# Kernel optimization log

Hardware: AMD Instinct MI355X
Metric: run time of the kernel (lower is better)

The kernel has to match this reference:

```python
import jax, jax.numpy as jnp
import numpy as np
import math

B, S, D, K = 8, 2048, 1024, 64
EPS = 1e-5

def _ln(x):
    m = jnp.mean(x, axis=-1, keepdims=True)
    v = jnp.mean((x - m) ** 2, axis=-1, keepdims=True)
    return (x - m) * jax.lax.rsqrt(v + EPS)

def setup_inputs() -> dict:
    key = jax.random.key(0)
    ks = jax.random.split(key, 14)
    s = 0.02
    return {
        "x":  jax.random.normal(ks[0], (B, S, D), dtype=jnp.float32),
        "Wk": jax.random.normal(ks[1], (D, K), dtype=jnp.float32) * s,
        "bk": jnp.zeros((K,), dtype=jnp.float32),
        "Wq": jax.random.normal(ks[2], (D, K), dtype=jnp.float32) * s,
        "bq": jnp.zeros((K,), dtype=jnp.float32),
        "Wv": jax.random.normal(ks[3], (D, D), dtype=jnp.float32) * s,
        "bv": jnp.zeros((D,), dtype=jnp.float32),
        "Wb": jax.random.normal(ks[4], (D, 1), dtype=jnp.float32) * s,
        "bb": jnp.zeros((1,), dtype=jnp.float32),
        "W1": jax.random.normal(ks[5], (D, D), dtype=jnp.float32) * s,
        "b1": jnp.zeros((D,), dtype=jnp.float32),
        "g1": jnp.ones((D,), dtype=jnp.float32),
        "be1": jnp.zeros((D,), dtype=jnp.float32),
    }

def reference(x, Wk, bk, Wq, bq, Wv, bv, Wb, bb, W1, b1, g1, be1):
    scale = 1.0 / math.sqrt(K)
    keys    = (jnp.einsum('bsd,dk->bsk', x, Wk) + bk) * scale   # [B,S,K]
    queries = jnp.einsum('bsd,dk->bsk', x, Wq) + bq             # [B,S,K]
    values  = jnp.einsum('bsd,de->bse', x, Wv) + bv             # [B,S,D]
    biases  = jnp.einsum('bsd,do->bso', x, Wb) + bb             # [B,S,1]
    # scores[b,i,j] = keys[b,i] . queries[b,j] + biases[b,i]
    scores = jax.nn.sigmoid(jnp.einsum('bik,bjk->bij', keys, queries) + biases)
    attention = jnp.einsum('bij,bjd->bid', scores, values)      # [B,S,D]
    res = _ln(x + attention) * g1 + be1
    feedforward = jax.nn.relu(jnp.einsum('bsd,de->bse', res, W1) + b1)
    return _ln(res + feedforward)
```

## Files before the change

### kernel.cpp

```cpp
#include <hip/hip_runtime.h>
#include <math.h>


typedef __bf16 bf16_t;
typedef __bf16 bf16x4_t __attribute__((ext_vector_type(4)));
typedef __bf16 bf16x8_t __attribute__((ext_vector_type(8)));
typedef float  f32x4    __attribute__((ext_vector_type(4)));

#define DEV static __device__ __forceinline__

DEV void gll16(const void* g, void* l) {
  __builtin_amdgcn_global_load_lds(
      (const __attribute__((address_space(1))) void*)g,
      (__attribute__((address_space(3))) void*)l, 16, 0, 0);
}

template <int MODE, int MFAST>
__global__ __launch_bounds__(512, 4) void gemm128n(
    const bf16_t* __restrict__ A, const bf16_t* __restrict__ B,
    bf16_t* __restrict__ C, int K, int lda, int ldb, int ldc,
    const float* __restrict__ aux0) {
  const int gx = gridDim.x, gy = gridDim.y;
  const int nwg = gx * gy;
  const int orig = blockIdx.x + gx * blockIdx.y;
  const int lid = (orig & 7) * (nwg >> 3) + (orig >> 3);
  const int bx = MFAST ? (lid / gy) : (lid % gx);
  const int by = MFAST ? (lid % gy) : (lid / gx);
  const int m0 = by * 256, n0 = bx * 128;

  __shared__ bf16_t SM[24576];
#define ASH(s) (&SM[(s) << 13])
#define BSH(s) (&SM[16384 + ((s) << 12)])

  const int tid = threadIdx.x;
  const int wid = tid >> 6, l = tid & 63;
  const int wr = wid >> 1, wc = wid & 1;
  const int lr = l & 15, lh = l >> 4;

  const int sRow = tid >> 2;
  const int sSl = (tid & 3) ^ ((tid >> 3) & 3);
  const bf16_t* Asrc = A + (long)(m0 + sRow) * lda + sSl * 8;
  const bf16_t* Bsrc = B + (long)(n0 + sRow) * ldb + sSl * 8;
  const long aStep = (long)128 * lda;

  const int sw = (lh ^ ((lr >> 1) & 3)) * 8;
  const int aOff = (wr * 64 + lr) * 32 + sw;
  const int bOff = (wc * 64 + lr) * 32 + sw;

  f32x4 acc[4][4] = {};
  const int NT = K >> 5;

  gll16(Asrc, ASH(0) + tid * 8);
  gll16(Asrc + aStep, ASH(0) + 4096 + tid * 8);
  gll16(Bsrc, BSH(0) + tid * 8);

  for (int h = 0; h < NT; ++h) {
    const int s = h & 1;
    asm volatile("s_waitcnt vmcnt(0)" ::: "memory");
    __builtin_amdgcn_sched_barrier(0);
    __builtin_amdgcn_s_barrier();
    if (h + 1 < NT) {
      const bf16_t* a_ = Asrc + (h + 1) * 32;
      const bf16_t* b_ = Bsrc + (h + 1) * 32;
      gll16(a_, ASH(s ^ 1) + tid * 8);
      gll16(a_ + aStep, ASH(s ^ 1) + 4096 + tid * 8);
      gll16(b_, BSH(s ^ 1) + tid * 8);
    }
    bf16x8_t aF[4], bF[4];
#pragma unroll
    for (int m = 0; m < 4; ++m) aF[m] = *(const bf16x8_t*)(ASH(s) + aOff + m * 512);
#pragma unroll
    for (int n = 0; n < 4; ++n) bF[n] = *(const bf16x8_t*)(BSH(s) + bOff + n * 512);
    asm volatile("s_waitcnt lgkmcnt(0)" ::: "memory");
    __builtin_amdgcn_sched_barrier(0);
    __builtin_amdgcn_s_setprio(1);
#pragma unroll
    for (int m = 0; m < 4; ++m)
#pragma unroll
      for (int n = 0; n < 4; ++n)
        acc[m][n] = __builtin_amdgcn_mfma_f32_16x16x32_bf16(aF[m], bF[n], acc[m][n], 0, 0, 0);
    __builtin_amdgcn_s_setprio(0);
  }

  const int rowb = m0 + wr * 64 + lh * 4;
  const int colb = n0 + wc * 64 + lr;
#pragma unroll
  for (int m = 0; m < 4; ++m)
#pragma unroll
    for (int n = 0; n < 4; ++n) {
      const f32x4 v = acc[m][n];
      const int cc = colb + n * 16;
#pragma unroll
      for (int r = 0; r < 4; ++r) {
        const int rr = rowb + m * 16 + r;
        const float val = v[r];
        if constexpr (MODE == 1) {
          C[(long)rr * ldc + cc] = (bf16_t)(val + aux0[rr]);
        } else {
          C[(long)rr * ldc + cc] = (bf16_t)fmaxf(val + aux0[cc], 0.0f);
        }
      }
    }
#undef ASH
#undef BSH
}

template <int MODE>
__global__ __launch_bounds__(512, 2) void gemm256p(
    const bf16_t* __restrict__ A, const bf16_t* __restrict__ B,
    bf16_t* __restrict__ C, int K, int lda, int ldb, int ldc,
    long sAb, long sBb, long sCb, const float* __restrict__ aux0) {
  const int gx = gridDim.x, gy = gridDim.y;
  const int gxy = gx * gy;
  const int nwg = gxy * (int)gridDim.z;
  const int orig = blockIdx.x + gx * blockIdx.y + gxy * blockIdx.z;
  const int lid = (orig & 7) * (nwg >> 3) + (orig >> 3);
  const int bz = lid / gxy;
  const int rem = lid - bz * gxy;
  const int bx = rem % gx;
  const int by = rem / gx;

  A += (long)bz * sAb;
  B += (long)bz * sBb;
  const int m0 = by * 256, n0 = bx * 256;

  __shared__ bf16_t SM[65536];
#define ASH(b, h) (&SM[(((b)*2 + (h)) << 13)])
#define BSH(b, h) (&SM[32768 + (((b)*2 + (h)) << 13)])

  const int tid = threadIdx.x;
  const int wid = tid >> 6, l = tid & 63;
  const int wr = wid >> 2, wc = wid & 3;
  const int lr = l & 15, lh = l >> 4;

  const int sRow = tid >> 2;
  const int sSl = (tid & 3) ^ ((tid >> 3) & 3);
  const bf16_t* Asrc = A + (long)(m0 + sRow) * lda + sSl * 8;
  const bf16_t* Bsrc = B + (long)(n0 + sRow) * ldb + sSl * 8;
  const long aStep = (long)128 * lda, bStep = (long)128 * ldb;

#define STAGE_A(b, h, kt) do { \
    const bf16_t* s_ = Asrc + (kt) * 64 + (h) * 32; \
    gll16(s_,         ASH(b, h) + tid * 8); \
    gll16(s_ + aStep, ASH(b, h) + 4096 + tid * 8); } while (0)
#define STAGE_B(b, h, kt) do { \
    const bf16_t* s_ = Bsrc + (kt) * 64 + (h) * 32; \
    gll16(s_,         BSH(b, h) + tid * 8); \
    gll16(s_ + bStep, BSH(b, h) + 4096 + tid * 8); } while (0)

  const int sw = (lh ^ ((lr >> 1) & 3)) * 8;
  const int aOff = (wr * 128 + lr) * 32 + sw;
  const int bOff = (wc * 64 + lr) * 32 + sw;

  f32x4 acc[8][4] = {};
  const int NT = K >> 6;

#define LGKM(n) do { \
    asm volatile("s_waitcnt lgkmcnt(" #n ")" ::: "memory"); \
    __builtin_amdgcn_sched_barrier(0); } while (0)
#define MFMA16(AS, BS, mo) do { \
    __builtin_amdgcn_s_setprio(1); \
    _Pragma("unroll") for (int m = 0; m < 4; ++m) \
    _Pragma("unroll") for (int n = 0; n < 4; ++n) \
      acc[m + (mo)][n] = __builtin_amdgcn_mfma_f32_16x16x32_bf16(AS[m], BS[n], acc[m + (mo)][n], 0, 0, 0); \
    __builtin_amdgcn_s_setprio(0); } while (0)

  STAGE_A(0, 0, 0); STAGE_B(0, 0, 0); STAGE_A(0, 1, 0); STAGE_B(0, 1, 0);
  asm volatile("s_waitcnt vmcnt(4)" ::: "memory");
  __builtin_amdgcn_s_barrier();

  bf16x8_t aA[4], aB[4], bA[4], bB[4];
#pragma unroll
  for (int n = 0; n < 4; ++n) bA[n] = *(const bf16x8_t*)(BSH(0, 0) + bOff + n * 512);
#pragma unroll
  for (int m = 0; m < 4; ++m) aA[m] = *(const bf16x8_t*)(ASH(0, 0) + aOff + m * 512);

  for (int t = 0; t < NT; ++t) {
    const int p = t & 1, q = p ^ 1;
    const bool pf = (t + 1 < NT);

#pragma unroll
    for (int m = 0; m < 4; ++m) aB[m] = *(const bf16x8_t*)(ASH(p, 0) + aOff + (m + 4) * 512);
    if (pf) STAGE_A(q, 0, t + 1);
    LGKM(4);
    MFMA16(aA, bA, 0);

    if (pf) {
      asm volatile("s_waitcnt vmcnt(2)" ::: "memory");
    } else {
      asm volatile("s_waitcnt vmcnt(0)" ::: "memory");
    }
    __builtin_amdgcn_sched_barrier(0);
    __builtin_amdgcn_s_barrier();
#pragma unroll
    for (int m = 0; m < 4; ++m) aA[m] = *(const bf16x8_t*)(ASH(p, 1) + aOff + m * 512);
#pragma unroll
    for (int n = 0; n < 4; ++n) bB[n] = *(const bf16x8_t*)(BSH(p, 1) + bOff + n * 512);
    if (pf) STAGE_B(q, 0, t + 1);
    LGKM(8);
    MFMA16(aB, bA, 4);

#pragma unroll
    for (int m = 0; m < 4; ++m) aB[m] = *(const bf16x8_t*)(ASH(p, 1) + aOff + (m + 4) * 512);
    if (pf) STAGE_A(q, 1, t + 1);
    LGKM(4);
    MFMA16(aA, bB, 0);

    if (pf) STAGE_B(q, 1, t + 1);
    asm volatile("s_waitcnt lgkmcnt(0)" ::: "memory");
    if (pf) {
      asm volatile("s_waitcnt vmcnt(4)" ::: "memory");
    }
    __builtin_amdgcn_sched_barrier(0);
    __builtin_amdgcn_s_barrier();
    if (pf) {
#pragma unroll
      for (int n = 0; n < 4; ++n) bA[n] = *(const bf16x8_t*)(BSH(q, 0) + bOff + n * 512);
#pragma unroll
      for (int m = 0; m < 4; ++m) aA[m] = *(const bf16x8_t*)(ASH(q, 0) + aOff + m * 512);
    }
    __builtin_amdgcn_sched_barrier(0);
    MFMA16(aB, bB, 4);
  }
#undef STAGE_A
#undef STAGE_B
#undef LGKM
#undef MFMA16

  bf16_t* Cb = C + (long)bz * sCb;
  const int rowb = m0 + wr * 128 + lh * 4;
  const int colb = n0 + wc * 64 + lr;
#pragma unroll
  for (int m = 0; m < 8; ++m)
#pragma unroll
    for (int n = 0; n < 4; ++n) {
      const f32x4 v = acc[m][n];
      const int cc = colb + n * 16;
#pragma unroll
      for (int r = 0; r < 4; ++r) {
        const int rr = rowb + m * 16 + r;
        Cb[(long)rr * ldc + cc] = (bf16_t)v[r];
      }
    }
#undef ASH
#undef BSH
}

__global__ __launch_bounds__(256) void scores128(
    const bf16_t* __restrict__ kq, bf16_t* __restrict__ C,
    const float* __restrict__ biases) {
  const int orig = blockIdx.x + 16 * blockIdx.y + 256 * blockIdx.z;
  const int lid = (orig & 7) * 256 + (orig >> 3);
  const int bz = lid >> 8;
  const int rem = lid & 255;
  const int bx = rem & 15, by = rem >> 4;

  const bf16_t* A = kq + (long)bz * 2048 * 128;
  const bf16_t* B = A + 64;
  const float* a0 = biases + (long)bz * 2048;
  const int m0 = by * 128, n0 = bx * 128;

  __shared__ bf16_t SM[16384];
#define ASH(h) (&SM[(h) << 12])
#define BSH(h) (&SM[8192 + ((h) << 12)])

  const int tid = threadIdx.x;
  const int w = tid >> 6, l = tid & 63;
  const int wr = w >> 1, wc = w & 1;
  const int lr = l & 15, lh = l >> 4;

  const int sRow = tid >> 2;
  const int sSl = ((tid & 3) ^ ((tid >> 3) & 3)) * 8;
  const bf16_t* As = A + (long)(m0 + sRow) * 128 + sSl;
  const bf16_t* Bs = B + (long)(n0 + sRow) * 128 + sSl;
#pragma unroll
  for (int h = 0; h < 2; ++h) {
    gll16(As + h * 32, ASH(h) + tid * 8);
    gll16(As + h * 32 + 64 * 128, ASH(h) + 2048 + tid * 8);
    gll16(Bs + h * 32, BSH(h) + tid * 8);
    gll16(Bs + h * 32 + 64 * 128, BSH(h) + 2048 + tid * 8);
  }
  asm volatile("s_waitcnt vmcnt(0)" ::: "memory");
  __builtin_amdgcn_s_barrier();

  const int sw = (lh ^ ((lr >> 1) & 3)) * 8;
  const int aOff = (wr * 64 + lr) * 32 + sw;
  const int bOff = (wc * 64 + lr) * 32 + sw;

  f32x4 acc[4][4] = {};
#pragma unroll
  for (int h = 0; h < 2; ++h) {
    bf16x8_t aF[4], bF[4];
#pragma unroll
    for (int m = 0; m < 4; ++m) aF[m] = *(const bf16x8_t*)(ASH(h) + aOff + m * 512);
#pragma unroll
    for (int n = 0; n < 4; ++n) bF[n] = *(const bf16x8_t*)(BSH(h) + bOff + n * 512);
#pragma unroll
    for (int m = 0; m < 4; ++m)
#pragma unroll
      for (int n = 0; n < 4; ++n)
        acc[m][n] = __builtin_amdgcn_mfma_f32_16x16x32_bf16(aF[m], bF[n], acc[m][n], 0, 0, 0);
  }

  __builtin_amdgcn_s_barrier();
  {
    const int rowb = (wr << 6) + (lh << 2);
    const int colb = (wc << 6) + lr;
#pragma unroll
    for (int m = 0; m < 4; ++m)
#pragma unroll
      for (int n = 0; n < 4; ++n) {
        const f32x4 v = acc[m][n];
        const int cl = colb + (n << 4);
#pragma unroll
        for (int r = 0; r < 4; ++r) {
          const int rl = rowb + (m << 4) + r;
          const float zz = v[r] + a0[m0 + rl];
          SM[rl * 128 + (cl ^ (lh << 4))] =
              (bf16_t)__builtin_amdgcn_rcpf(1.0f + __expf(-zz));
        }
      }
    __syncthreads();
    bf16_t* Cb = C + (long)bz * 2048 * 2048;
    const int chunk = tid & 15, rsub = tid >> 4;
#pragma unroll
    for (int pp = 0; pp < 8; ++pp) {
      const int rl = pp * 16 + rsub;
      const int sc = chunk ^ (((rl >> 2) & 3) << 1);
      const bf16x8_t vv = *(const bf16x8_t*)&SM[rl * 128 + sc * 8];
      *(bf16x8_t*)&Cb[(long)(m0 + rl) * 2048 + n0 + chunk * 8] = vv;
    }
  }
#undef ASH
#undef BSH
}

__global__ __launch_bounds__(256) void kq_thin(
    const bf16_t* __restrict__ A, const bf16_t* __restrict__ B,
    bf16_t* __restrict__ C,
    const float* __restrict__ bk, const float* __restrict__ bq) {
  const int m0 = blockIdx.x * 64;

  __shared__ bf16_t SM[12288];
#define ASH(b) (&SM[(b) << 11])
#define BSH(b) (&SM[4096 + ((b) << 12)])

  const int tid = threadIdx.x;
  const int w = tid >> 6, l = tid & 63;
  const int lr = l & 15, lh = l >> 4;

  const int sRow = tid >> 2;
  const int sSl = (tid & 3) ^ ((tid >> 3) & 3);
  const bf16_t* Asrc = A + (long)(m0 + sRow) * 1024 + sSl * 8;
  const bf16_t* Bsrc0 = B + (long)sRow * 1024 + sSl * 8;
  const bf16_t* Bsrc1 = B + (long)(64 + sRow) * 1024 + sSl * 8;

  const int sw = (lh ^ ((lr >> 1) & 3)) * 8;
  const int aOff = (w * 16 + lr) * 32 + sw;

  f32x4 acc[8] = {};

  auto stage = [&](int buf, int k0) {
    gll16(Asrc + k0, ASH(buf) + tid * 8);
    gll16(Bsrc0 + k0, BSH(buf) + tid * 8);
    gll16(Bsrc1 + k0, BSH(buf) + 2048 + tid * 8);
  };

  stage(0, 0);
  __syncthreads();
  int cur = 0;

  for (int k0 = 0; k0 < 1024; k0 += 32) {
    if (k0 + 32 < 1024) stage(cur ^ 1, k0 + 32);

    const bf16x8_t aF = *(const bf16x8_t*)(ASH(cur) + aOff);
    bf16x8_t bF[8];
#pragma unroll
    for (int j = 0; j < 8; ++j)
      bF[j] = *(const bf16x8_t*)(BSH(cur) + (j * 16 + lr) * 32 + sw);
#pragma unroll
    for (int j = 0; j < 8; ++j)
      acc[j] = __builtin_amdgcn_mfma_f32_16x16x32_bf16(aF, bF[j], acc[j], 0, 0, 0);

    __syncthreads();
    cur ^= 1;
  }

  {
#pragma unroll
    for (int j = 0; j < 8; ++j) {
      const f32x4 v = acc[j];
      const int cl = j * 16 + lr;
      const float b = (cl < 64) ? bk[cl] : bq[cl - 64];
      const float s = (cl < 64) ? 0.125f : 1.0f;
#pragma unroll
      for (int r = 0; r < 4; ++r) {
        const int rl = w * 16 + lh * 4 + r;
        SM[rl * 128 + (cl ^ (lh << 4))] = (bf16_t)((v[r] + b) * s);
      }
    }
    __syncthreads();
    const int chunk = tid & 15, rsub = tid >> 4;
#pragma unroll
    for (int pp = 0; pp < 4; ++pp) {
      const int rl = pp * 16 + rsub;
      const int sc = chunk ^ (((rl >> 2) & 3) << 1);
      const bf16x8_t vv = *(const bf16x8_t*)&SM[rl * 128 + sc * 8];
      *(bf16x8_t*)&C[(long)(m0 + rl) * 128 + chunk * 8] = vv;
    }
  }
#undef ASH
#undef BSH
}

__global__ __launch_bounds__(256) void cast_bias_kernel(
    const float* __restrict__ x, const float* __restrict__ Wb,
    const float* __restrict__ bb, bf16_t* __restrict__ x_bf,
    float* __restrict__ biases) {
  const int r = blockIdx.x * 4 + (threadIdx.x >> 6);
  const int l = threadIdx.x & 63;
  const float* xr = x + (long)r * 1024;
  bf16_t* orow = x_bf + (long)r * 1024;
  float s = 0.f;
#pragma unroll
  for (int i = 0; i < 4; ++i) {
    const int off = l * 4 + i * 256;
    const float4 v = *(const float4*)(xr + off);
    const float4 w = *(const float4*)(Wb + off);
    s += v.x * w.x + v.y * w.y + v.z * w.z + v.w * w.w;
    bf16x4_t o;
    o[0] = (bf16_t)v.x; o[1] = (bf16_t)v.y; o[2] = (bf16_t)v.z; o[3] = (bf16_t)v.w;
    *(bf16x4_t*)(orow + off) = o;
  }
#pragma unroll
  for (int off = 1; off < 64; off <<= 1) s += __shfl_xor(s, off);
  if (l == 0) biases[r] = s + bb[0];
}

__global__ __launch_bounds__(256) void transpose_all(
    const float* __restrict__ Wk, const float* __restrict__ Wq,
    const float* __restrict__ Wv, const float* __restrict__ W1,
    bf16_t* __restrict__ Wkqt, bf16_t* __restrict__ Wvt,
    bf16_t* __restrict__ W1t) {
  int b = blockIdx.x;
  const float* in;
  bf16_t* out;
  int R, C, c0, r0;
  if (b < 1024) {
    in = Wv; out = Wvt; R = 1024; C = 1024;
    c0 = (b & 31) * 32; r0 = (b >> 5) * 32;
  } else if (b < 2048) {
    b -= 1024; in = W1; out = W1t; R = 1024; C = 1024;
    c0 = (b & 31) * 32; r0 = (b >> 5) * 32;
  } else if (b < 2112) {
    b -= 2048; in = Wk; out = Wkqt; R = 1024; C = 64;
    c0 = (b & 1) * 32; r0 = (b >> 1) * 32;
  } else {
    b -= 2112; in = Wq; out = Wkqt + 64 * 1024; R = 1024; C = 64;
    c0 = (b & 1) * 32; r0 = (b >> 1) * 32;
  }
  __shared__ float t[32][33];
  const int tx = threadIdx.x & 31, ty = threadIdx.x >> 5;
#pragma unroll
  for (int i = 0; i < 4; ++i) {
    const int rl = ty * 4 + i;
    t[rl][tx] = in[(long)(r0 + rl) * C + c0 + tx];
  }
  __syncthreads();
#pragma unroll
  for (int i = 0; i < 4; ++i) {
    const int rl = ty * 4 + i;
    out[(long)(c0 + rl) * R + r0 + tx] = (bf16_t)t[tx][rl];
  }
}

__global__ __launch_bounds__(256) void ln1_kernel(
    const bf16_t* __restrict__ x, const bf16_t* __restrict__ attn,
    const float* __restrict__ g, const float* __restrict__ be,
    bf16_t* __restrict__ res) {
  const int w = threadIdx.x >> 6, l = threadIdx.x & 63;
  const long r = (long)blockIdx.x * 4 + w;
  const bf16_t* xr = x + r * 1024;
  const bf16_t* ar = attn + r * 1024;
  float y[16];
  float s = 0.f, ss = 0.f;
#pragma unroll
  for (int h = 0; h < 2; ++h) {
    const int base = h * 512 + l * 8;
    const bf16x8_t xv = *(const bf16x8_t*)(xr + base);
    const bf16x8_t av = *(const bf16x8_t*)(ar + base);
#pragma unroll
    for (int j = 0; j < 8; ++j) {
      const float yy = (float)xv[j] + (float)av[j];
      y[h * 8 + j] = yy;
      s += yy; ss += yy * yy;
    }
  }
#pragma unroll
  for (int off = 1; off < 64; off <<= 1) {
    s += __shfl_xor(s, off);
    ss += __shfl_xor(ss, off);
  }
  const float mean = s * (1.0f / 1024.0f);
  const float rs = rsqrtf(ss * (1.0f / 1024.0f) - mean * mean + 1e-5f);
  bf16_t* orow = res + r * 1024;
#pragma unroll
  for (int h = 0; h < 2; ++h) {
    const int base = h * 512 + l * 8;
    bf16x8_t o;
#pragma unroll
    for (int j = 0; j < 8; ++j)
      o[j] = (bf16_t)((y[h * 8 + j] - mean) * rs * g[base + j] + be[base + j]);
    *(bf16x8_t*)(orow + base) = o;
  }
}

__global__ __launch_bounds__(256) void ln2_kernel(
    const bf16_t* __restrict__ res, const bf16_t* __restrict__ hh,
    float* __restrict__ out) {
  const int w = threadIdx.x >> 6, l = threadIdx.x & 63;
  const long r = (long)blockIdx.x * 4 + w;
  const bf16_t* rr = res + r * 1024;
  const bf16_t* hr = hh + r * 1024;
  float y[16];
  float s = 0.f, ss = 0.f;
#pragma unroll
  for (int h = 0; h < 2; ++h) {
    const int base = h * 512 + l * 8;
    const bf16x8_t rv = *(const bf16x8_t*)(rr + base);
    const bf16x8_t hv = *(const bf16x8_t*)(hr + base);
#pragma unroll
    for (int j = 0; j < 8; ++j) {
      const float yy = (float)rv[j] + (float)hv[j];
      y[h * 8 + j] = yy;
      s += yy; ss += yy * yy;
    }
  }
#pragma unroll
  for (int off = 1; off < 64; off <<= 1) {
    s += __shfl_xor(s, off);
    ss += __shfl_xor(ss, off);
  }
  const float mean = s * (1.0f / 1024.0f);
  const float rs = rsqrtf(ss * (1.0f / 1024.0f) - mean * mean + 1e-5f);
  float* orow = out + r * 1024;
#pragma unroll
  for (int h = 0; h < 2; ++h) {
    const int base = h * 512 + l * 8;
    float4 o1, o2;
    o1.x = (y[h * 8 + 0] - mean) * rs; o1.y = (y[h * 8 + 1] - mean) * rs;
    o1.z = (y[h * 8 + 2] - mean) * rs; o1.w = (y[h * 8 + 3] - mean) * rs;
    o2.x = (y[h * 8 + 4] - mean) * rs; o2.y = (y[h * 8 + 5] - mean) * rs;
    o2.z = (y[h * 8 + 6] - mean) * rs; o2.w = (y[h * 8 + 7] - mean) * rs;
    *(float4*)(orow + base) = o1;
    *(float4*)(orow + base + 4) = o2;
  }
}

extern "C" void kernel_launch(void* const* d_in, const int* in_sizes, int n_in,
                              void* d_out, int out_size, void* d_ws, size_t ws_size,
                              hipStream_t stream) {
  const float* x   = (const float*)d_in[0];
  const float* Wk  = (const float*)d_in[1];
  const float* bk  = (const float*)d_in[2];
  const float* Wq  = (const float*)d_in[3];
  const float* bq  = (const float*)d_in[4];
  const float* Wv  = (const float*)d_in[5];
  const float* bv  = (const float*)d_in[6];
  const float* Wb  = (const float*)d_in[7];
  const float* bb  = (const float*)d_in[8];
  const float* W1  = (const float*)d_in[9];
  const float* b1  = (const float*)d_in[10];
  const float* g1  = (const float*)d_in[11];
  const float* be1 = (const float*)d_in[12];
  float* out = (float*)d_out;

  char* ws = (char*)d_ws;
  bf16_t* x_bf    = (bf16_t*)(ws + 0);
  bf16_t* vt_bf   = (bf16_t*)(ws + 33554432);
  bf16_t* kq_bf   = (bf16_t*)(ws + 67108864);
  bf16_t* Wkqt    = (bf16_t*)(ws + 71303168);
  bf16_t* Wvt     = (bf16_t*)(ws + 71565312);
  bf16_t* W1t     = (bf16_t*)(ws + 73662464);
  float*  biases  = (float*) (ws + 75759616);
  bf16_t* scores  = (bf16_t*)(ws + 75825152);
  bf16_t* attn_bf = (bf16_t*)(ws + 142934016);
  bf16_t* res_bf  = (bf16_t*)(ws + 176488448);
  bf16_t* h_bf    = attn_bf;

  cast_bias_kernel<<<4096, 256, 0, stream>>>(x, Wb, bb, x_bf, biases);
  transpose_all<<<2176, 256, 0, stream>>>(Wk, Wq, Wv, W1, Wkqt, Wvt, W1t);

  kq_thin<<<256, 256, 0, stream>>>(x_bf, Wkqt, kq_bf, bk, bq);

  gemm128n<1, 1><<<dim3(128, 4), 512, 0, stream>>>(
      Wvt, x_bf, vt_bf, 1024, 1024, 1024, 16384, bv);

  scores128<<<dim3(16, 16, 8), 256, 0, stream>>>(kq_bf, scores, biases);

  gemm256p<3><<<dim3(4, 8, 8), 512, 0, stream>>>(
      scores, vt_bf, attn_bf, 2048, 2048, 16384, 1024,
      2048L * 2048, 2048, 2048L * 1024, nullptr);

  ln1_kernel<<<4096, 256, 0, stream>>>(x_bf, attn_bf, g1, be1, res_bf);

  gemm128n<4, 0><<<dim3(8, 64), 512, 0, stream>>>(
      res_bf, W1t, h_bf, 1024, 1024, 1024, 1024, b1);

  ln2_kernel<<<4096, 256, 0, stream>>>(res_bf, h_bf, out);
}
```

Baseline: 235.5 us.

## Fuse feed-forward GEMM with final LayerNorm and merge prep kernels

```diff
diff --git a/kernel.cpp b/kernel.cpp
--- a/kernel.cpp
+++ b/kernel.cpp
@@ -13,6 +13,122 @@
   __builtin_amdgcn_global_load_lds(
       (const __attribute__((address_space(1))) void*)g,
       (__attribute__((address_space(3))) void*)l, 16, 0, 0);
+}
+
+__global__ __launch_bounds__(512, 2) void ff_rowln(
+    const bf16_t* __restrict__ A, const bf16_t* __restrict__ B,
+    const float* __restrict__ b1, float* __restrict__ out) {
+  const int m0 = blockIdx.x * 64;
+
+  __shared__ bf16_t SM[69632];
+#define ASH(s) (&SM[(s) << 11])
+#define BSH(s) (&SM[4096 + ((s) << 15)])
+  float* SM32 = (float*)SM;
+
+  const int tid = threadIdx.x;
+  const int wc = tid >> 6, l = tid & 63;
+  const int lr = l & 15, lh = l >> 4;
+
+  const int gRow = tid >> 2;
+  const int gSl = ((tid & 3) ^ ((tid >> 3) & 3)) * 8;
+  const bf16_t* Asrc = A + (long)(m0 + gRow) * 1024 + gSl;
+  const bf16_t* Bsrc = B + (long)gRow * 1024 + gSl;
+
+  const int sw = (lh ^ ((lr >> 1) & 3)) * 8;
+
+  f32x4 acc[4][8] = {};
+
+#define STAGE(s, kt) do { \
+    if (tid < 256) gll16(Asrc + (kt) * 32, ASH(s) + tid * 8); \
+    _Pragma("unroll") for (int r = 0; r < 8; ++r) \
+      gll16(Bsrc + (long)r * 131072 + (kt) * 32, BSH(s) + (r * 512 + tid) * 8); \
+  } while (0)
+
+  STAGE(0, 0);
+  for (int kt = 0; kt < 32; ++kt) {
+    const int s = kt & 1;
+    asm volatile("s_waitcnt vmcnt(0)" ::: "memory");
+    __builtin_amdgcn_sched_barrier(0);
+    __builtin_amdgcn_s_barrier();
+    if (kt + 1 < 32) STAGE(s ^ 1, kt + 1);
+    bf16x8_t aF[4], bF[8];
+#pragma unroll
+    for (int m = 0; m < 4; ++m)
+      aF[m] = *(const bf16x8_t*)(ASH(s) + (m * 16 + lr) * 32 + sw);
+#pragma unroll
+    for (int n = 0; n < 8; ++n)
+      bF[n] = *(const bf16x8_t*)(BSH(s) + (wc * 128 + n * 16 + lr) * 32 + sw);
+    asm volatile("s_waitcnt lgkmcnt(0)" ::: "memory");
+    __builtin_amdgcn_sched_barrier(0);
+    __builtin_amdgcn_s_setprio(1);
+#pragma unroll
+    for (int m = 0; m < 4; ++m)
+#pragma unroll
+      for (int n = 0; n < 8; ++n)
+        acc[m][n] = __builtin_amdgcn_mfma_f32_16x16x32_bf16(aF[m], bF[n], acc[m][n], 0, 0, 0);
+    __builtin_amdgcn_s_setprio(0);
+  }
+#undef STAGE
+
+  const int ecol0 = wc * 128 + lr;
+#pragma unroll
+  for (int half = 0; half < 2; ++half) {
+    __builtin_amdgcn_s_barrier();
+#pragma unroll
+    for (int mm = 0; mm < 2; ++mm) {
+#pragma unroll
+      for (int n = 0; n < 8; ++n) {
+        const int col = ecol0 + n * 16;
+        const float bb = b1[col];
+        const f32x4 v = acc[half * 2 + mm][n];
+#pragma unroll
+        for (int r = 0; r < 4; ++r) {
+          const int row32 = mm * 16 + lh * 4 + r;
+          const int chunk = (col >> 2) ^ (row32 & 15);
+          SM32[row32 * 1024 + chunk * 4 + (col & 3)] = fmaxf(v[r] + bb, 0.f);
+        }
+      }
+    }
+    __builtin_amdgcn_s_barrier();
+    const int row = tid >> 4, seg = tid & 15;
+    const long grow = m0 + half * 32 + row;
+    const bf16_t* resp = A + grow * 1024 + seg * 64;
+    float y[64];
+    float s = 0.f, ss = 0.f;
+#pragma unroll
+    for (int j = 0; j < 8; ++j) {
+      const bf16x8_t rv = *(const bf16x8_t*)(resp + j * 8);
+      const int c0 = seg * 16 + 2 * j;
+      const f32x4 h0 = *(const f32x4*)&SM32[row * 1024 + ((c0 ^ (row & 15)) << 2)];
+      const f32x4 h1 = *(const f32x4*)&SM32[row * 1024 + (((c0 + 1) ^ (row & 15)) << 2)];
+#pragma unroll
+      for (int k = 0; k < 4; ++k) {
+        const float y0 = h0[k] + (float)rv[k];
+        y[j * 8 + k] = y0; s += y0; ss += y0 * y0;
+        const float y1 = h1[k] + (float)rv[4 + k];
+        y[j * 8 + 4 + k] = y1; s += y1; ss += y1 * y1;
+      }
+    }
+#pragma unroll
+    for (int off = 1; off < 16; off <<= 1) {
+      s += __shfl_xor(s, off);
+      ss += __shfl_xor(ss, off);
+    }
+    const float mean = s * (1.0f / 1024.0f);
+    const float rstd = rsqrtf(ss * (1.0f / 1024.0f) - mean * mean + 1e-5f);
+    float4* op = (float4*)(out + grow * 1024 + seg * 64);
+#pragma unroll
+    for (int j = 0; j < 16; ++j) {
+      float4 o;
+      o.x = (y[j * 4 + 0] - mean) * rstd;
+      o.y = (y[j * 4 + 1] - mean) * rstd;
+      o.z = (y[j * 4 + 2] - mean) * rstd;
+      o.w = (y[j * 4 + 3] - mean) * rstd;
+      op[j] = o;
+    }
+  }
+#undef ASH
+#undef BSH
 }
 
 template <int MODE, int MFAST>
@@ -93,12 +209,7 @@
 #pragma unroll
       for (int r = 0; r < 4; ++r) {
         const int rr = rowb + m * 16 + r;
-        const float val = v[r];
-        if constexpr (MODE == 1) {
-          C[(long)rr * ldc + cc] = (bf16_t)(val + aux0[rr]);
-        } else {
-          C[(long)rr * ldc + cc] = (bf16_t)fmaxf(val + aux0[cc], 0.0f);
-        }
+        C[(long)rr * ldc + cc] = (bf16_t)(v[r] + aux0[rr]);
       }
     }
 #undef ASH
@@ -413,53 +524,53 @@
 #undef BSH
 }
 
-__global__ __launch_bounds__(256) void cast_bias_kernel(
+__global__ __launch_bounds__(256) void prep(
     const float* __restrict__ x, const float* __restrict__ Wb,
     const float* __restrict__ bb, bf16_t* __restrict__ x_bf,
-    float* __restrict__ biases) {
-  const int r = blockIdx.x * 4 + (threadIdx.x >> 6);
-  const int l = threadIdx.x & 63;
-  const float* xr = x + (long)r * 1024;
-  bf16_t* orow = x_bf + (long)r * 1024;
-  float s = 0.f;
-#pragma unroll
-  for (int i = 0; i < 4; ++i) {
-    const int off = l * 4 + i * 256;
-    const float4 v = *(const float4*)(xr + off);
-    const float4 w = *(const float4*)(Wb + off);
-    s += v.x * w.x + v.y * w.y + v.z * w.z + v.w * w.w;
-    bf16x4_t o;
-    o[0] = (bf16_t)v.x; o[1] = (bf16_t)v.y; o[2] = (bf16_t)v.z; o[3] = (bf16_t)v.w;
-    *(bf16x4_t*)(orow + off) = o;
-  }
-#pragma unroll
-  for (int off = 1; off < 64; off <<= 1) s += __shfl_xor(s, off);
-  if (l == 0) biases[r] = s + bb[0];
-}
-
-__global__ __launch_bounds__(256) void transpose_all(
+    float* __restrict__ biases,
     const float* __restrict__ Wk, const float* __restrict__ Wq,
     const float* __restrict__ Wv, const float* __restrict__ W1,
     bf16_t* __restrict__ Wkqt, bf16_t* __restrict__ Wvt,
     bf16_t* __restrict__ W1t) {
-  int b = blockIdx.x;
+  __shared__ float t[32][33];
+  if (blockIdx.x < 4096) {
+    const int r = blockIdx.x * 4 + (threadIdx.x >> 6);
+    const int l = threadIdx.x & 63;
+    const float* xr = x + (long)r * 1024;
+    bf16_t* orow = x_bf + (long)r * 1024;
+    float s = 0.f;
+#pragma unroll
+    for (int i = 0; i < 4; ++i) {
+      const int off = l * 4 + i * 256;
+      const float4 v = *(const float4*)(xr + off);
+      const float4 w = *(const float4*)(Wb + off);
+      s += v.x * w.x + v.y * w.y + v.z * w.z + v.w * w.w;
+      bf16x4_t o;
+      o[0] = (bf16_t)v.x; o[1] = (bf16_t)v.y; o[2] = (bf16_t)v.z; o[3] = (bf16_t)v.w;
+      *(bf16x4_t*)(orow + off) = o;
+    }
+#pragma unroll
+    for (int off = 1; off < 64; off <<= 1) s += __shfl_xor(s, off);
+    if (l == 0) biases[r] = s + bb[0];
+    return;
+  }
+  int b = blockIdx.x - 4096;
   const float* in;
   bf16_t* out;
-  int R, C, c0, r0;
+  int R = 1024, C, c0, r0;
   if (b < 1024) {
-    in = Wv; out = Wvt; R = 1024; C = 1024;
+    in = Wv; out = Wvt; C = 1024;
     c0 = (b & 31) * 32; r0 = (b >> 5) * 32;
   } else if (b < 2048) {
-    b -= 1024; in = W1; out = W1t; R = 1024; C = 1024;
+    b -= 1024; in = W1; out = W1t; C = 1024;
     c0 = (b & 31) * 32; r0 = (b >> 5) * 32;
   } else if (b < 2112) {
-    b -= 2048; in = Wk; out = Wkqt; R = 1024; C = 64;
+    b -= 2048; in = Wk; out = Wkqt; C = 64;
     c0 = (b & 1) * 32; r0 = (b >> 1) * 32;
   } else {
-    b -= 2112; in = Wq; out = Wkqt + 64 * 1024; R = 1024; C = 64;
+    b -= 2112; in = Wq; out = Wkqt + 64 * 1024; C = 64;
     c0 = (b & 1) * 32; r0 = (b >> 1) * 32;
   }
-  __shared__ float t[32][33];
   const int tx = threadIdx.x & 31, ty = threadIdx.x >> 5;
 #pragma unroll
   for (int i = 0; i < 4; ++i) {
@@ -512,48 +623,6 @@
     for (int j = 0; j < 8; ++j)
       o[j] = (bf16_t)((y[h * 8 + j] - mean) * rs * g[base + j] + be[base + j]);
     *(bf16x8_t*)(orow + base) = o;
-  }
-}
-
-__global__ __launch_bounds__(256) void ln2_kernel(
-    const bf16_t* __restrict__ res, const bf16_t* __restrict__ hh,
-    float* __restrict__ out) {
-  const int w = threadIdx.x >> 6, l = threadIdx.x & 63;
-  const long r = (long)blockIdx.x * 4 + w;
-  const bf16_t* rr = res + r * 1024;
-  const bf16_t* hr = hh + r * 1024;
-  float y[16];
-  float s = 0.f, ss = 0.f;
-#pragma unroll
-  for (int h = 0; h < 2; ++h) {
-    const int base = h * 512 + l * 8;
-    const bf16x8_t rv = *(const bf16x8_t*)(rr + base);
-    const bf16x8_t hv = *(const bf16x8_t*)(hr + base);
-#pragma unroll
-    for (int j = 0; j < 8; ++j) {
-      const float yy = (float)rv[j] + (float)hv[j];
-      y[h * 8 + j] = yy;
-      s += yy; ss += yy * yy;
-    }
-  }
-#pragma unroll
-  for (int off = 1; off < 64; off <<= 1) {
-    s += __shfl_xor(s, off);
-    ss += __shfl_xor(ss, off);
-  }
-  const float mean = s * (1.0f / 1024.0f);
-  const float rs = rsqrtf(ss * (1.0f / 1024.0f) - mean * mean + 1e-5f);
-  float* orow = out + r * 1024;
-#pragma unroll
-  for (int h = 0; h < 2; ++h) {
-    const int base = h * 512 + l * 8;
-    float4 o1, o2;
-    o1.x = (y[h * 8 + 0] - mean) * rs; o1.y = (y[h * 8 + 1] - mean) * rs;
-    o1.z = (y[h * 8 + 2] - mean) * rs; o1.w = (y[h * 8 + 3] - mean) * rs;
-    o2.x = (y[h * 8 + 4] - mean) * rs; o2.y = (y[h * 8 + 5] - mean) * rs;
-    o2.z = (y[h * 8 + 6] - mean) * rs; o2.w = (y[h * 8 + 7] - mean) * rs;
-    *(float4*)(orow + base) = o1;
-    *(float4*)(orow + base + 4) = o2;
   }
 }
 
@@ -586,10 +655,9 @@
   bf16_t* scores  = (bf16_t*)(ws + 75825152);
   bf16_t* attn_bf = (bf16_t*)(ws + 142934016);
   bf16_t* res_bf  = (bf16_t*)(ws + 176488448);
-  bf16_t* h_bf    = attn_bf;
-
-  cast_bias_kernel<<<4096, 256, 0, stream>>>(x, Wb, bb, x_bf, biases);
-  transpose_all<<<2176, 256, 0, stream>>>(Wk, Wq, Wv, W1, Wkqt, Wvt, W1t);
+
+  prep<<<6272, 256, 0, stream>>>(x, Wb, bb, x_bf, biases,
+                                 Wk, Wq, Wv, W1, Wkqt, Wvt, W1t);
 
   kq_thin<<<256, 256, 0, stream>>>(x_bf, Wkqt, kq_bf, bk, bq);
 
@@ -604,8 +672,5 @@
 
   ln1_kernel<<<4096, 256, 0, stream>>>(x_bf, attn_bf, g1, be1, res_bf);
 
-  gemm128n<4, 0><<<dim3(8, 64), 512, 0, stream>>>(
-      res_bf, W1t, h_bf, 1024, 1024, 1024, 1024, b1);
-
-  ln2_kernel<<<4096, 256, 0, stream>>>(res_bf, h_bf, out);
-}
+  ff_rowln<<<256, 512, 0, stream>>>(res_bf, W1t, b1, out);
+}
```

After: 246.7 us. 1.05x slower.
